# Kernel tuning notes

Hardware: AMD Instinct MI355X
Metric: run time of the kernel (lower is better)

Reference implementation:

```python
import jax, jax.numpy as jnp
import numpy as np

N_U, N_P, E = 200000, 50000, 500000
D_U, D_P, H, OUT = 100, 50, 128, 1
BN_EPS = 1e-5


def _lin(k, dout, din):
    s = 1.0 / np.sqrt(din)
    kw, kb = jax.random.split(k)
    W = jax.random.uniform(kw, (dout, din), jnp.float32, -s, s)
    b = jax.random.uniform(kb, (dout,), jnp.float32, -s, s)
    return W, b


def setup_inputs() -> dict:
    key = jax.random.key(0)
    ks = jax.random.split(key, 12)
    x_u = jax.random.normal(ks[0], (N_U, D_U), jnp.float32)
    x_p = jax.random.normal(ks[1], (N_P, D_P), jnp.float32)
    src = jax.random.randint(ks[2], (E,), 0, N_U, jnp.int64) if jax.config.jax_enable_x64 else jax.random.randint(ks[2], (E,), 0, N_U)
    dst = jax.random.randint(ks[3], (E,), N_U, N_U + N_P)
    edge_index = jnp.stack([src, dst]).astype(jnp.int32)
    W_u, b_u = _lin(ks[4], H, D_U)
    W_p, b_p = _lin(ks[5], H, D_P)
    W1l, b1l = _lin(ks[6], H, H)   # SAGEConv lin_l (aggregated neighbors, carries bias)
    W1r, _ = _lin(ks[7], H, H)     # SAGEConv lin_r (root, no bias)
    W2l, b2l = _lin(ks[8], H, H)
    W2r, _ = _lin(ks[9], H, H)
    W_out, b_out = _lin(ks[10], OUT, H)
    return dict(x_u=x_u, x_p=x_p, edge_index=edge_index,
                W_u=W_u, b_u=b_u, W_p=W_p, b_p=b_p,
                W1l=W1l, b1l=b1l, W1r=W1r,
                g1=jnp.ones((H,), jnp.float32), be1=jnp.zeros((H,), jnp.float32),
                W2l=W2l, b2l=b2l, W2r=W2r,
                g2=jnp.ones((H,), jnp.float32), be2=jnp.zeros((H,), jnp.float32),
                W_out=W_out, b_out=b_out)


def reference(x_u, x_p, edge_index, W_u, b_u, W_p, b_p,
              W1l, b1l, W1r, g1, be1, W2l, b2l, W2r, g2, be2,
              W_out, b_out):
    N = x_u.shape[0] + x_p.shape[0]
    # input projections + relu, then concat users/products -> [N, H]
    x = jnp.concatenate([jax.nn.relu(x_u @ W_u.T + b_u),
                         jax.nn.relu(x_p @ W_p.T + b_p)], axis=0)
    # to_undirected: add reversed edges (bipartite => no duplicates)
    src = jnp.concatenate([edge_index[0], edge_index[1]])
    dst = jnp.concatenate([edge_index[1], edge_index[0]])
    deg = jnp.maximum(jax.ops.segment_sum(jnp.ones_like(dst, jnp.float32), dst, num_segments=N), 1.0)

    def sage(h, Wl, bl, Wr):
        # mean aggregation of neighbor features, scatter by dst
        mean = jax.ops.segment_sum(h[src], dst, num_segments=N) / deg[:, None]
        return mean @ Wl.T + bl + h @ Wr.T

    def bn(h, g, b):
        m = h.mean(0)
        v = h.var(0)  # biased variance, as used for normalization in torch BN
        return (h - m) * jax.lax.rsqrt(v + BN_EPS) * g + b

    h1 = jax.nn.relu(bn(sage(x, W1l, b1l, W1r), g1, be1))   # dropout = identity (eval)
    h2 = jax.nn.relu(bn(sage(h1, W2l, b2l, W2r), g2, be2)) + x
    return h2[: x_u.shape[0]] @ W_out.T + b_out
```

## Files before the change

kernel.cpp:

```cpp
#include <hip/hip_runtime.h>
#include <hip/hip_bf16.h>
#include <cstdint>
#include <cstddef>

#define NT   250000
#define NUU  200000
#define NPP  50000
#define EG   500000
#define E2   1000000
#define HD   128
#define NBLK_SCAN 977
#define NTILES 1954

#define X_OFF     0ull
#define R1_OFF    64000000ull
#define R2_OFF    128000000ull
#define CNT_OFF   179200000ull
#define SPART_OFF 180200000ull
#define SS_OFF    180265536ull
#define RPTR_OFF  180267584ull
#define BSUM_OFF  181267588ull
#define BMAT_OFF  181271504ull
#define COL_OFF   181451728ull
#define WS_NEED   185451728ull

typedef __hip_bfloat16 bf16;
typedef __attribute__((ext_vector_type(8))) short short8v;
typedef __attribute__((ext_vector_type(4))) float f32x4;

__device__ inline float bflo(unsigned u) { return __builtin_bit_cast(float, u << 16); }
__device__ inline float bfhi(unsigned u) { return __builtin_bit_cast(float, u & 0xffff0000u); }
__device__ inline float b2f(short s) { return __builtin_bit_cast(float, ((unsigned)(unsigned short)s) << 16); }
__device__ inline unsigned short f2bf(float f) { return __builtin_bit_cast(unsigned short, __float2bfloat16(f)); }

__global__ __launch_bounds__(256) void k_zero(int* __restrict__ p, int n) {
    for (int i = blockIdx.x * 256 + threadIdx.x; i < n; i += gridDim.x * 256) p[i] = 0;
}

__global__ __launch_bounds__(256) void k_count(const int* __restrict__ ei, int* __restrict__ cnt) {
    for (int e = blockIdx.x * 256 + threadIdx.x; e < E2; e += gridDim.x * 256) {
        int d = (e < EG) ? ei[e + EG] : ei[e - EG];
        atomicAdd(&cnt[d], 1);
    }
}

__global__ __launch_bounds__(256) void k_scan1(const int* __restrict__ cnt, int* __restrict__ bsum) {
    __shared__ int lds[256];
    int i = blockIdx.x * 256 + threadIdx.x;
    int v = (i < NT) ? cnt[i] : 0;
    lds[threadIdx.x] = v; __syncthreads();
    for (int s = 128; s > 0; s >>= 1) {
        if (threadIdx.x < s) lds[threadIdx.x] += lds[threadIdx.x + s];
        __syncthreads();
    }
    if (threadIdx.x == 0) bsum[blockIdx.x] = lds[0];
}

__global__ __launch_bounds__(1024) void k_scan2(int* __restrict__ bsum) {
    __shared__ int lds[1024];
    int i = threadIdx.x;
    int v = (i < NBLK_SCAN) ? bsum[i] : 0;
    lds[i] = v; __syncthreads();
    for (int off = 1; off < 1024; off <<= 1) {
        int t = (i >= off) ? lds[i - off] : 0;
        __syncthreads();
        lds[i] += t;
        __syncthreads();
    }
    if (i < NBLK_SCAN) bsum[i] = lds[i] - v;
}

__global__ __launch_bounds__(256) void k_scan3(const int* __restrict__ cnt, const int* __restrict__ bsum,
                                               int* __restrict__ rp) {
    __shared__ int lds[256];
    int i = blockIdx.x * 256 + threadIdx.x;
    int v = (i < NT) ? cnt[i] : 0;
    lds[threadIdx.x] = v; __syncthreads();
    for (int off = 1; off < 256; off <<= 1) {
        int t = (threadIdx.x >= off) ? lds[threadIdx.x - off] : 0;
        __syncthreads();
        lds[threadIdx.x] += t;
        __syncthreads();
    }
    if (i < NT) rp[i] = bsum[blockIdx.x] + lds[threadIdx.x] - v;
    if (i == 0 && blockIdx.x == 0) rp[NT] = E2;
}

__global__ __launch_bounds__(256) void k_fill(const int* __restrict__ ei, const int* __restrict__ rp,
                                              int* __restrict__ fill, int* __restrict__ col) {
    for (int e = blockIdx.x * 256 + threadIdx.x; e < E2; e += gridDim.x * 256) {
        int s = ei[e];
        int d = (e < EG) ? ei[e + EG] : ei[e - EG];
        int slot = rp[d] + atomicAdd(&fill[d], 1);
        col[slot] = s;
    }
}

__global__ __launch_bounds__(256) void k_wcvt(const float* __restrict__ W1l, const float* __restrict__ W1r,
                                              const float* __restrict__ W2l, const float* __restrict__ W2r,
                                              const float* __restrict__ Wu, const float* __restrict__ Wp,
                                              bf16* __restrict__ B) {
    int i = blockIdx.x * 256 + threadIdx.x;
    if (i < 65536) {
        int layer = i >> 15, rem = i & 32767, o = rem >> 8, k = rem & 255;
        const float* W = layer ? ((k < 128) ? W2l : W2r) : ((k < 128) ? W1l : W1r);
        B[i] = __float2bfloat16(W[o * 128 + (k & 127)]);
    } else if (i < 81920) {
        int rem = i - 65536, o = rem >> 7, k = rem & 127;
        B[i] = __float2bfloat16((k < 100) ? Wu[o * 100 + k] : 0.f);
    } else if (i < 90112) {
        int rem = i - 81920, o = rem >> 6, k = rem & 63;
        B[i] = __float2bfloat16((k < 50) ? Wp[o * 50 + k] : 0.f);
    }
}

template<int DIN, int KPAD>
__global__ __launch_bounds__(256) void k_projm(const float* __restrict__ in, const bf16* __restrict__ Bp,
                                               const float* __restrict__ bias, bf16* __restrict__ outp,
                                               int nrows, int rowbase) {
    const int lane = threadIdx.x & 63;
    const int wid = threadIdx.x >> 6;
    const int wr = wid >> 1, wc = wid & 1;
    const int r15 = lane & 15, l4 = lane >> 4;
    const int tb = blockIdx.x * 128;
    constexpr int NKS = KPAD / 32;

    f32x4 acc[4][4] = {};
#pragma unroll
    for (int ks = 0; ks < NKS; ks++) {
        int kk = ks * 32 + l4 * 8;
        short8v a[4], b[4];
#pragma unroll
        for (int m = 0; m < 4; m++) {
            int r = tb + wr * 64 + m * 16 + r15;
            if (r > nrows - 1) r = nrows - 1;
            const float* src = in + (size_t)r * DIN + kk;
            short8v v;
            if (ks * 32 + 32 <= DIN) {
                const float2* s2 = (const float2*)src;
                float2 f0 = s2[0], f1 = s2[1], f2 = s2[2], f3 = s2[3];
                v[0] = (short)f2bf(f0.x); v[1] = (short)f2bf(f0.y);
                v[2] = (short)f2bf(f1.x); v[3] = (short)f2bf(f1.y);
                v[4] = (short)f2bf(f2.x); v[5] = (short)f2bf(f2.y);
                v[6] = (short)f2bf(f3.x); v[7] = (short)f2bf(f3.y);
            } else {
#pragma unroll
                for (int j = 0; j < 8; j++) {
                    float f = (kk + j < DIN) ? src[j] : 0.f;
                    v[j] = (short)f2bf(f);
                }
            }
            a[m] = v;
        }
#pragma unroll
        for (int n = 0; n < 4; n++) {
            int c = wc * 64 + n * 16 + r15;
            b[n] = *(const short8v*)(Bp + (size_t)c * KPAD + kk);
        }
#pragma unroll
        for (int m = 0; m < 4; m++)
#pragma unroll
            for (int n = 0; n < 4; n++)
                acc[m][n] = __builtin_amdgcn_mfma_f32_16x16x32_bf16(a[m], b[n], acc[m][n], 0, 0, 0);
    }
    float bcol[4];
#pragma unroll
    for (int n = 0; n < 4; n++) bcol[n] = bias[wc * 64 + n * 16 + r15];
#pragma unroll
    for (int m = 0; m < 4; m++)
#pragma unroll
        for (int n = 0; n < 4; n++)
#pragma unroll
            for (int g = 0; g < 4; g++) {
                int row = tb + wr * 64 + m * 16 + l4 * 4 + g;
                if (row < nrows) {
                    float v = fmaxf(acc[m][n][g] + bcol[n], 0.f);
                    outp[(size_t)(rowbase + row) * HD + wc * 64 + n * 16 + r15] = __float2bfloat16(v);
                }
            }
}

template<bool NORM>
__global__ __launch_bounds__(256) void k_gemm(const bf16* __restrict__ hin, const float* __restrict__ ssv,
                                              const int* __restrict__ rp, const int* __restrict__ col,
                                              const bf16* __restrict__ Bmat, const float* __restrict__ blv,
                                              bf16* __restrict__ outp, float* __restrict__ spart,
                                              int store_n) {
    int g = blockIdx.x / 5, pos = blockIdx.x % 5;
    int tile = (pos < 4) ? (g * 4 + pos) : (1563 + g);
    if (pos < 4 && tile > 1562) return;

    __shared__ unsigned int mrow[8192];
    const int tid = threadIdx.x;
    const int lane = tid & 63;
    const int wid = tid >> 6;
    const int g16 = lane >> 4, l16 = lane & 15;
    const int tb = tile * 128;
    const int wnb = wid * 32;
    const int fo = l16 * 8;

    float sv[8], tv[8];
    if (NORM) {
#pragma unroll
        for (int j = 0; j < 8; j++) { sv[j] = ssv[fo + j]; tv[j] = ssv[HD + fo + j]; }
    }

    int rpv = 0;
    if (lane <= 32) rpv = rp[min(tb + wnb + lane, NT)];

    for (int t = 0; t < 4; t++) {
        int nlA = wnb + t * 8 + g16;
        int nlB = nlA + 4;
        int a0 = __shfl(rpv, t * 8 + g16),     a1 = __shfl(rpv, t * 8 + g16 + 1);
        int b0 = __shfl(rpv, t * 8 + g16 + 4), b1 = __shfl(rpv, t * 8 + g16 + 5);
        if (tb + nlA >= NT) { a0 = 0; a1 = 0; }
        if (tb + nlB >= NT) { b0 = 0; b1 = 0; }
        float accA[8] = {}, accB[8] = {};
        int pA = a0, pB = b0;
        while (pA < a1 || pB < b1) {
            int iA0 = (pA     < a1) ? pA     : 0;
            int iA1 = (pA + 1 < a1) ? pA + 1 : 0;
            int iA2 = (pA + 2 < a1) ? pA + 2 : 0;
            int iA3 = (pA + 3 < a1) ? pA + 3 : 0;
            int iB0 = (pB     < b1) ? pB     : 0;
            int iB1 = (pB + 1 < b1) ? pB + 1 : 0;
            int iB2 = (pB + 2 < b1) ? pB + 2 : 0;
            int iB3 = (pB + 3 < b1) ? pB + 3 : 0;
            int cA0 = col[iA0], cA1 = col[iA1], cA2 = col[iA2], cA3 = col[iA3];
            int cB0 = col[iB0], cB1 = col[iB1], cB2 = col[iB2], cB3 = col[iB3];
            short8v uA0 = *(const short8v*)(hin + (size_t)cA0 * HD + fo);
            short8v uA1 = *(const short8v*)(hin + (size_t)cA1 * HD + fo);
            short8v uA2 = *(const short8v*)(hin + (size_t)cA2 * HD + fo);
            short8v uA3 = *(const short8v*)(hin + (size_t)cA3 * HD + fo);
            short8v uB0 = *(const short8v*)(hin + (size_t)cB0 * HD + fo);
            short8v uB1 = *(const short8v*)(hin + (size_t)cB1 * HD + fo);
            short8v uB2 = *(const short8v*)(hin + (size_t)cB2 * HD + fo);
            short8v uB3 = *(const short8v*)(hin + (size_t)cB3 * HD + fo);
            float mA0 = (pA     < a1) ? 1.f : 0.f;
            float mA1 = (pA + 1 < a1) ? 1.f : 0.f;
            float mA2 = (pA + 2 < a1) ? 1.f : 0.f;
            float mA3 = (pA + 3 < a1) ? 1.f : 0.f;
            float mB0 = (pB     < b1) ? 1.f : 0.f;
            float mB1 = (pB + 1 < b1) ? 1.f : 0.f;
            float mB2 = (pB + 2 < b1) ? 1.f : 0.f;
            float mB3 = (pB + 3 < b1) ? 1.f : 0.f;
#pragma unroll
            for (int j = 0; j < 8; j++) {
                float vA0 = b2f(uA0[j]), vA1 = b2f(uA1[j]), vA2 = b2f(uA2[j]), vA3 = b2f(uA3[j]);
                float vB0 = b2f(uB0[j]), vB1 = b2f(uB1[j]), vB2 = b2f(uB2[j]), vB3 = b2f(uB3[j]);
                if (NORM) {
                    vA0 = fmaxf(fmaf(vA0, sv[j], tv[j]), 0.f);
                    vA1 = fmaxf(fmaf(vA1, sv[j], tv[j]), 0.f);
                    vA2 = fmaxf(fmaf(vA2, sv[j], tv[j]), 0.f);
                    vA3 = fmaxf(fmaf(vA3, sv[j], tv[j]), 0.f);
                    vB0 = fmaxf(fmaf(vB0, sv[j], tv[j]), 0.f);
                    vB1 = fmaxf(fmaf(vB1, sv[j], tv[j]), 0.f);
                    vB2 = fmaxf(fmaf(vB2, sv[j], tv[j]), 0.f);
                    vB3 = fmaxf(fmaf(vB3, sv[j], tv[j]), 0.f);
                }
                accA[j] += mA0 * vA0 + mA1 * vA1 + mA2 * vA2 + mA3 * vA3;
                accB[j] += mB0 * vB0 + mB1 * vB1 + mB2 * vB2 + mB3 * vB3;
            }
            pA += 4; pB += 4;
        }
        float invA = 1.f / (float)max(a1 - a0, 1);
        float invB = 1.f / (float)max(b1 - b0, 1);
        short8v wA, wB;
#pragma unroll
        for (int j = 0; j < 8; j++) {
            wA[j] = (short)f2bf(accA[j] * invA);
            wB[j] = (short)f2bf(accB[j] * invB);
        }
        int byteA = (nlA * 256 + l16 * 16) ^ ((nlA & 7) << 4);
        int byteB = (nlB * 256 + l16 * 16) ^ ((nlB & 7) << 4);
        *(short8v*)((char*)mrow + byteA) = wA;
        *(short8v*)((char*)mrow + byteB) = wB;
    }
    __syncthreads();

    const int wr = wid >> 1, wc = wid & 1;
    const int r15 = lane & 15, l4 = lane >> 4;
    f32x4 acc[4][4] = {};
#pragma unroll
    for (int ks = 0; ks < 8; ks++) {
        short8v a[4], b[4];
        if (ks < 4) {
            int kb = ks * 64 + l4 * 16;
#pragma unroll
            for (int m = 0; m < 4; m++) {
                int r = wr * 64 + m * 16 + r15;
                int byte = (r * 256 + kb) ^ ((r & 7) << 4);
                a[m] = *(const short8v*)((const char*)mrow + byte);
            }
        } else {
            int k2 = (ks - 4) * 32 + l4 * 8;
            float sv2[8], tv2[8];
            if (NORM) {
#pragma unroll
                for (int j = 0; j < 8; j++) { sv2[j] = ssv[k2 + j]; tv2[j] = ssv[HD + k2 + j]; }
            }
#pragma unroll
            for (int m = 0; m < 4; m++) {
                int r = tb + wr * 64 + m * 16 + r15; if (r > NT - 1) r = NT - 1;
                short8v v = *(const short8v*)(hin + (size_t)r * HD + k2);
                if (NORM) {
#pragma unroll
                    for (int j = 0; j < 8; j++) {
                        float f = b2f(v[j]);
                        f = fmaxf(fmaf(f, sv2[j], tv2[j]), 0.f);
                        v[j] = (short)f2bf(f);
                    }
                }
                a[m] = v;
            }
        }
#pragma unroll
        for (int n = 0; n < 4; n++) {
            int c = wc * 64 + n * 16 + r15;
            b[n] = *(const short8v*)(Bmat + (size_t)c * 256 + ks * 32 + l4 * 8);
        }
#pragma unroll
        for (int m = 0; m < 4; m++)
#pragma unroll
            for (int n = 0; n < 4; n++)
                acc[m][n] = __builtin_amdgcn_mfma_f32_16x16x32_bf16(a[m], b[n], acc[m][n], 0, 0, 0);
    }

    float bcol[4];
#pragma unroll
    for (int n = 0; n < 4; n++) bcol[n] = blv[wc * 64 + n * 16 + r15];
    float ls[4] = {0.f, 0.f, 0.f, 0.f}, lq[4] = {0.f, 0.f, 0.f, 0.f};
#pragma unroll
    for (int m = 0; m < 4; m++)
#pragma unroll
        for (int n = 0; n < 4; n++)
#pragma unroll
            for (int gg = 0; gg < 4; gg++) {
                int row = tb + wr * 64 + m * 16 + l4 * 4 + gg;
                float v = acc[m][n][gg] + bcol[n];
                if (row < NT) { ls[n] += v; lq[n] += v * v; }
                if (row < store_n)
                    outp[(size_t)row * HD + wc * 64 + n * 16 + r15] = __float2bfloat16(v);
            }
    int part = (tile & 31) * 256;
#pragma unroll
    for (int n = 0; n < 4; n++) {
        float s = ls[n], q2 = lq[n];
        s  += __shfl_xor(s, 16);  s  += __shfl_xor(s, 32);
        q2 += __shfl_xor(q2, 16); q2 += __shfl_xor(q2, 32);
        if (l4 == 0) {
            int c = wc * 64 + n * 16 + r15;
            atomicAdd(&spart[part + c], s);
            atomicAdd(&spart[part + 128 + c], q2);
        }
    }
}

__global__ void k_fin(const float* __restrict__ sp, const float* __restrict__ g,
                      const float* __restrict__ be, float* __restrict__ ssout) {
    int j = threadIdx.x;
    float m = 0.f, q = 0.f;
    for (int i = 0; i < 32; i++) { m += sp[i * 256 + j]; q += sp[i * 256 + 128 + j]; }
    m *= (1.f / (float)NT);
    q = q * (1.f / (float)NT) - m * m;
    float s = g[j] * rsqrtf(q + 1e-5f);
    ssout[j] = s;
    ssout[HD + j] = be[j] - m * s;
}

__global__ __launch_bounds__(256) void k_out(const bf16* __restrict__ r2, const float* __restrict__ ss,
                                             const bf16* __restrict__ x, const float* __restrict__ wout,
                                             const float* __restrict__ bout, float* __restrict__ outp) {
    int lane = threadIdx.x & 63;
    int wid = (blockIdx.x * blockDim.x + threadIdx.x) >> 6;
    int nwv = (gridDim.x * blockDim.x) >> 6;
    int j0 = lane * 2;
    float s0 = ss[j0],       s1 = ss[j0 + 1];
    float t0 = ss[HD + j0],  t1 = ss[HD + j0 + 1];
    float w0 = wout[j0], w1 = wout[j0 + 1];
    float bo = bout[0];
    for (int r = wid; r < NUU; r += nwv) {
        unsigned ua = *(const unsigned*)(r2 + (size_t)r * HD + j0);
        unsigned ux = *(const unsigned*)(x + (size_t)r * HD + j0);
        float h0 = fmaxf(fmaf(bflo(ua), s0, t0), 0.f) + bflo(ux);
        float h1 = fmaxf(fmaf(bfhi(ua), s1, t1), 0.f) + bfhi(ux);
        float acc = h0 * w0 + h1 * w1;
#pragma unroll
        for (int off = 32; off; off >>= 1) acc += __shfl_down(acc, off);
        if (lane == 0) outp[r] = acc + bo;
    }
}

extern "C" void kernel_launch(void* const* d_in, const int* in_sizes, int n_in,
                              void* d_out, int out_size, void* d_ws, size_t ws_size,
                              hipStream_t stream) {
    const float* x_u = (const float*)d_in[0];
    const float* x_p = (const float*)d_in[1];
    const int*   ei  = (const int*)d_in[2];
    const float* W_u = (const float*)d_in[3];
    const float* b_u = (const float*)d_in[4];
    const float* W_p = (const float*)d_in[5];
    const float* b_p = (const float*)d_in[6];
    const float* W1l = (const float*)d_in[7];
    const float* b1l = (const float*)d_in[8];
    const float* W1r = (const float*)d_in[9];
    const float* g1  = (const float*)d_in[10];
    const float* be1 = (const float*)d_in[11];
    const float* W2l = (const float*)d_in[12];
    const float* b2l = (const float*)d_in[13];
    const float* W2r = (const float*)d_in[14];
    const float* g2  = (const float*)d_in[15];
    const float* be2 = (const float*)d_in[16];
    const float* Wout = (const float*)d_in[17];
    const float* bout = (const float*)d_in[18];

    float* out = (float*)d_out;

    if (ws_size < WS_NEED) {
        k_zero<<<512, 256, 0, stream>>>((int*)d_out, out_size);
        return;
    }

    char* ws = (char*)d_ws;
    bf16* X      = (bf16*)(ws + X_OFF);
    bf16* R1     = (bf16*)(ws + R1_OFF);
    bf16* R2     = (bf16*)(ws + R2_OFF);
    int*  cnt    = (int*)(ws + CNT_OFF);
    float* spart = (float*)(ws + SPART_OFF);
    float* ssbuf = (float*)(ws + SS_OFF);
    int*  rp     = (int*)(ws + RPTR_OFF);
    int*  bsum   = (int*)(ws + BSUM_OFF);
    bf16* Bmat   = (bf16*)(ws + BMAT_OFF);
    int*  col    = (int*)(ws + COL_OFF);

    k_zero<<<1043, 256, 0, stream>>>(cnt, 266896);
    k_wcvt<<<352, 256, 0, stream>>>(W1l, W1r, W2l, W2r, W_u, W_p, Bmat);

    k_count<<<1024, 256, 0, stream>>>(ei, cnt);
    k_scan1<<<NBLK_SCAN, 256, 0, stream>>>(cnt, bsum);
    k_scan2<<<1, 1024, 0, stream>>>(bsum);
    k_scan3<<<NBLK_SCAN, 256, 0, stream>>>(cnt, bsum, rp);
    k_zero<<<977, 256, 0, stream>>>(cnt, NT);
    k_fill<<<1024, 256, 0, stream>>>(ei, rp, cnt, col);

    k_projm<100, 128><<<1563, 256, 0, stream>>>(x_u, Bmat + 65536, b_u, X, NUU, 0);
    k_projm<50, 64><<<391, 256, 0, stream>>>(x_p, Bmat + 81920, b_p, X, NPP, NUU);

    k_gemm<false><<<1955, 256, 0, stream>>>(X, nullptr, rp, col, Bmat, b1l, R1, spart, NT);
    k_fin<<<1, 128, 0, stream>>>(spart, g1, be1, ssbuf);

    k_gemm<true><<<1955, 256, 0, stream>>>(R1, ssbuf, rp, col, Bmat + 32768, b2l, R2, spart + 8192, NUU);
    k_fin<<<1, 128, 0, stream>>>(spart + 8192, g2, be2, ssbuf + 256);

    k_out<<<2048, 256, 0, stream>>>(R2, ssbuf + 256, X, Wout, bout, out);
}
```

Measured before the change: 452.6 us.

## Split fused gather-GEMM into separate SpMM and dense MFMA kernels

```diff
diff --git a/kernel.cpp b/kernel.cpp
--- a/kernel.cpp
+++ b/kernel.cpp
@@ -10,7 +10,6 @@
 #define E2   1000000
 #define HD   128
 #define NBLK_SCAN 977
-#define NTILES 1954
 
 #define X_OFF     0ull
 #define R1_OFF    64000000ull
@@ -23,6 +22,18 @@
 #define BMAT_OFF  181271504ull
 #define COL_OFF   181451728ull
 #define WS_NEED   185451728ull
+
+#define CNT2_OFF   0ull
+#define SPART2_OFF 1000000ull
+#define SS2_OFF    1065536ull
+#define RPTR2_OFF  1067584ull
+#define BSUM2_OFF  2067588ull
+#define BMAT2_OFF  2071504ull
+#define COL2_OFF   2251728ull
+#define X2_OFF     6251728ull
+#define R1B_OFF    70251728ull
+#define C2_OFF     134251728ull
+#define WS_SPLIT   198251728ull
 
 typedef __hip_bfloat16 bf16;
 typedef __attribute__((ext_vector_type(8))) short short8v;
@@ -137,12 +148,21 @@
             const float* src = in + (size_t)r * DIN + kk;
             short8v v;
             if (ks * 32 + 32 <= DIN) {
-                const float2* s2 = (const float2*)src;
-                float2 f0 = s2[0], f1 = s2[1], f2 = s2[2], f3 = s2[3];
-                v[0] = (short)f2bf(f0.x); v[1] = (short)f2bf(f0.y);
-                v[2] = (short)f2bf(f1.x); v[3] = (short)f2bf(f1.y);
-                v[4] = (short)f2bf(f2.x); v[5] = (short)f2bf(f2.y);
-                v[6] = (short)f2bf(f3.x); v[7] = (short)f2bf(f3.y);
+                if constexpr (DIN % 4 == 0) {
+                    const float4* s4 = (const float4*)src;
+                    float4 f0 = s4[0], f1 = s4[1];
+                    v[0] = (short)f2bf(f0.x); v[1] = (short)f2bf(f0.y);
+                    v[2] = (short)f2bf(f0.z); v[3] = (short)f2bf(f0.w);
+                    v[4] = (short)f2bf(f1.x); v[5] = (short)f2bf(f1.y);
+                    v[6] = (short)f2bf(f1.z); v[7] = (short)f2bf(f1.w);
+                } else {
+                    const float2* s2 = (const float2*)src;
+                    float2 f0 = s2[0], f1 = s2[1], f2 = s2[2], f3 = s2[3];
+                    v[0] = (short)f2bf(f0.x); v[1] = (short)f2bf(f0.y);
+                    v[2] = (short)f2bf(f1.x); v[3] = (short)f2bf(f1.y);
+                    v[4] = (short)f2bf(f2.x); v[5] = (short)f2bf(f2.y);
+                    v[6] = (short)f2bf(f3.x); v[7] = (short)f2bf(f3.y);
+                }
             } else {
 #pragma unroll
                 for (int j = 0; j < 8; j++) {
@@ -178,6 +198,140 @@
                     outp[(size_t)(rowbase + row) * HD + wc * 64 + n * 16 + r15] = __float2bfloat16(v);
                 }
             }
+}
+
+template<bool NORM>
+__global__ __launch_bounds__(256) void k_spmm(const bf16* __restrict__ hin, const float* __restrict__ ssv,
+                                              const int* __restrict__ rp, const int* __restrict__ col,
+                                              bf16* __restrict__ M) {
+    const int tid = threadIdx.x;
+    const int gid = tid >> 4, l16 = tid & 15;
+    const int fo = l16 * 8;
+    float sv[8], tv[8];
+    if (NORM) {
+#pragma unroll
+        for (int j = 0; j < 8; j++) { sv[j] = ssv[fo + j]; tv[j] = ssv[HD + fo + j]; }
+    }
+    for (int n = blockIdx.x * 16 + gid; n < NT; n += gridDim.x * 16) {
+        int s0 = rp[n], s1 = rp[n + 1];
+        float a[8] = {};
+        for (int p = s0; p < s1; p += 4) {
+            int i1 = min(p + 1, s1 - 1), i2 = min(p + 2, s1 - 1), i3 = min(p + 3, s1 - 1);
+            int c0 = col[p], c1 = col[i1], c2 = col[i2], c3 = col[i3];
+            short8v u0 = *(const short8v*)(hin + (size_t)c0 * HD + fo);
+            short8v u1 = *(const short8v*)(hin + (size_t)c1 * HD + fo);
+            short8v u2 = *(const short8v*)(hin + (size_t)c2 * HD + fo);
+            short8v u3 = *(const short8v*)(hin + (size_t)c3 * HD + fo);
+            float m1 = (p + 1 < s1) ? 1.f : 0.f;
+            float m2 = (p + 2 < s1) ? 1.f : 0.f;
+            float m3 = (p + 3 < s1) ? 1.f : 0.f;
+#pragma unroll
+            for (int j = 0; j < 8; j++) {
+                float v0 = b2f(u0[j]), v1 = b2f(u1[j]), v2 = b2f(u2[j]), v3 = b2f(u3[j]);
+                if (NORM) {
+                    v0 = fmaxf(fmaf(v0, sv[j], tv[j]), 0.f);
+                    v1 = fmaxf(fmaf(v1, sv[j], tv[j]), 0.f);
+                    v2 = fmaxf(fmaf(v2, sv[j], tv[j]), 0.f);
+                    v3 = fmaxf(fmaf(v3, sv[j], tv[j]), 0.f);
+                }
+                a[j] += v0 + m1 * v1 + m2 * v2 + m3 * v3;
+            }
+        }
+        float inv = 1.f / (float)max(s1 - s0, 1);
+        short8v w;
+#pragma unroll
+        for (int j = 0; j < 8; j++) w[j] = (short)f2bf(a[j] * inv);
+        *(short8v*)(M + (size_t)n * HD + fo) = w;
+    }
+}
+
+template<bool NORM>
+__global__ __launch_bounds__(256) void k_dense(const bf16* __restrict__ Min, const bf16* __restrict__ hin,
+                                               const float* __restrict__ ssv,
+                                               const bf16* __restrict__ Bmat, const float* __restrict__ blv,
+                                               bf16* __restrict__ outp, float* __restrict__ spart,
+                                               int store_n) {
+    const int lane = threadIdx.x & 63;
+    const int wid = threadIdx.x >> 6;
+    const int wr = wid >> 1, wc = wid & 1;
+    const int r15 = lane & 15, l4 = lane >> 4;
+    const int tb = blockIdx.x * 128;
+
+    f32x4 acc[4][4] = {};
+#pragma unroll
+    for (int ks = 0; ks < 8; ks++) {
+        short8v a[4], b[4];
+        if (ks < 4) {
+            int k0 = ks * 32 + l4 * 8;
+#pragma unroll
+            for (int m = 0; m < 4; m++) {
+                int r = tb + wr * 64 + m * 16 + r15; if (r > NT - 1) r = NT - 1;
+                a[m] = *(const short8v*)(Min + (size_t)r * HD + k0);
+            }
+        } else {
+            int k2 = (ks - 4) * 32 + l4 * 8;
+            float sv2[8], tv2[8];
+            if (NORM) {
+#pragma unroll
+                for (int j = 0; j < 8; j++) { sv2[j] = ssv[k2 + j]; tv2[j] = ssv[HD + k2 + j]; }
+            }
+#pragma unroll
+            for (int m = 0; m < 4; m++) {
+                int r = tb + wr * 64 + m * 16 + r15; if (r > NT - 1) r = NT - 1;
+                short8v v = *(const short8v*)(hin + (size_t)r * HD + k2);
+                if (NORM) {
+#pragma unroll
+                    for (int j = 0; j < 8; j++) {
+                        float f = b2f(v[j]);
+                        f = fmaxf(fmaf(f, sv2[j], tv2[j]), 0.f);
+                        v[j] = (short)f2bf(f);
+                    }
+                }
+                a[m] = v;
+            }
+        }
+#pragma unroll
+        for (int n = 0; n < 4; n++) {
+            int c = wc * 64 + n * 16 + r15;
+            b[n] = *(const short8v*)(Bmat + (size_t)c * 256 + ks * 32 + l4 * 8);
+        }
+#pragma unroll
+        for (int m = 0; m < 4; m++)
+#pragma unroll
+            for (int n = 0; n < 4; n++)
+                acc[m][n] = __builtin_amdgcn_mfma_f32_16x16x32_bf16(a[m], b[n], acc[m][n], 0, 0, 0);
+    }
+
+    __syncthreads();
+
+    float bcol[4];
+#pragma unroll
+    for (int n = 0; n < 4; n++) bcol[n] = blv[wc * 64 + n * 16 + r15];
+    float ls[4] = {0.f, 0.f, 0.f, 0.f}, lq[4] = {0.f, 0.f, 0.f, 0.f};
+#pragma unroll
+    for (int m = 0; m < 4; m++)
+#pragma unroll
+        for (int n = 0; n < 4; n++)
+#pragma unroll
+            for (int gg = 0; gg < 4; gg++) {
+                int row = tb + wr * 64 + m * 16 + l4 * 4 + gg;
+                float v = acc[m][n][gg] + bcol[n];
+                if (row < NT) { ls[n] += v; lq[n] += v * v; }
+                if (row < store_n)
+                    outp[(size_t)row * HD + wc * 64 + n * 16 + r15] = __float2bfloat16(v);
+            }
+    int part = (blockIdx.x & 31) * 256;
+#pragma unroll
+    for (int n = 0; n < 4; n++) {
+        float s = ls[n], q2 = lq[n];
+        s  += __shfl_xor(s, 16);  s  += __shfl_xor(s, 32);
+        q2 += __shfl_xor(q2, 16); q2 += __shfl_xor(q2, 32);
+        if (l4 == 0) {
+            int c = wc * 64 + n * 16 + r15;
+            atomicAdd(&spart[part + c], s);
+            atomicAdd(&spart[part + 128 + c], q2);
+        }
+    }
 }
 
 template<bool NORM>
@@ -204,7 +358,6 @@
 #pragma unroll
         for (int j = 0; j < 8; j++) { sv[j] = ssv[fo + j]; tv[j] = ssv[HD + fo + j]; }
     }
-
     int rpv = 0;
     if (lane <= 32) rpv = rp[min(tb + wnb + lane, NT)];
 
@@ -372,22 +525,31 @@
                                              const bf16* __restrict__ x, const float* __restrict__ wout,
                                              const float* __restrict__ bout, float* __restrict__ outp) {
     int lane = threadIdx.x & 63;
-    int wid = (blockIdx.x * blockDim.x + threadIdx.x) >> 6;
+    int wv = (blockIdx.x * blockDim.x + threadIdx.x) >> 6;
     int nwv = (gridDim.x * blockDim.x) >> 6;
-    int j0 = lane * 2;
-    float s0 = ss[j0],       s1 = ss[j0 + 1];
-    float t0 = ss[HD + j0],  t1 = ss[HD + j0 + 1];
-    float w0 = wout[j0], w1 = wout[j0 + 1];
+    int g16 = lane >> 4, l16 = lane & 15;
+    int fo = l16 * 8;
+    float s8[8], t8[8], w8[8];
+#pragma unroll
+    for (int j = 0; j < 8; j++) {
+        s8[j] = ss[fo + j]; t8[j] = ss[HD + fo + j]; w8[j] = wout[fo + j];
+    }
     float bo = bout[0];
-    for (int r = wid; r < NUU; r += nwv) {
-        unsigned ua = *(const unsigned*)(r2 + (size_t)r * HD + j0);
-        unsigned ux = *(const unsigned*)(x + (size_t)r * HD + j0);
-        float h0 = fmaxf(fmaf(bflo(ua), s0, t0), 0.f) + bflo(ux);
-        float h1 = fmaxf(fmaf(bfhi(ua), s1, t1), 0.f) + bfhi(ux);
-        float acc = h0 * w0 + h1 * w1;
-#pragma unroll
-        for (int off = 32; off; off >>= 1) acc += __shfl_down(acc, off);
-        if (lane == 0) outp[r] = acc + bo;
+    for (int r0 = wv * 4; r0 < NUU; r0 += nwv * 4) {
+        int row = r0 + g16;
+        short8v a  = *(const short8v*)(r2 + (size_t)row * HD + fo);
+        short8v xx = *(const short8v*)(x  + (size_t)row * HD + fo);
+        float acc = 0.f;
+#pragma unroll
+        for (int j = 0; j < 8; j++) {
+            float h = fmaxf(fmaf(b2f(a[j]), s8[j], t8[j]), 0.f) + b2f(xx[j]);
+            acc += h * w8[j];
+        }
+        acc += __shfl_xor(acc, 1);
+        acc += __shfl_xor(acc, 2);
+        acc += __shfl_xor(acc, 4);
+        acc += __shfl_xor(acc, 8);
+        if (l16 == 0) outp[row] = acc + bo;
     }
 }
 
@@ -413,15 +575,50 @@
     const float* be2 = (const float*)d_in[16];
     const float* Wout = (const float*)d_in[17];
     const float* bout = (const float*)d_in[18];
-
     float* out = (float*)d_out;
+    char* ws = (char*)d_ws;
+
+    if (ws_size >= WS_SPLIT) {
+        int*  cnt    = (int*)(ws + CNT2_OFF);
+        float* spart = (float*)(ws + SPART2_OFF);
+        float* ssbuf = (float*)(ws + SS2_OFF);
+        int*  rp     = (int*)(ws + RPTR2_OFF);
+        int*  bsum   = (int*)(ws + BSUM2_OFF);
+        bf16* Bmat   = (bf16*)(ws + BMAT2_OFF);
+        int*  col    = (int*)(ws + COL2_OFF);
+        bf16* X      = (bf16*)(ws + X2_OFF);
+        bf16* R1     = (bf16*)(ws + R1B_OFF);
+        bf16* MC     = (bf16*)(ws + C2_OFF);
+
+        k_zero<<<1043, 256, 0, stream>>>(cnt, 266896);
+        k_wcvt<<<352, 256, 0, stream>>>(W1l, W1r, W2l, W2r, W_u, W_p, Bmat);
+
+        k_count<<<1024, 256, 0, stream>>>(ei, cnt);
+        k_scan1<<<NBLK_SCAN, 256, 0, stream>>>(cnt, bsum);
+        k_scan2<<<1, 1024, 0, stream>>>(bsum);
+        k_scan3<<<NBLK_SCAN, 256, 0, stream>>>(cnt, bsum, rp);
+        k_zero<<<977, 256, 0, stream>>>(cnt, NT);
+        k_fill<<<1024, 256, 0, stream>>>(ei, rp, cnt, col);
+
+        k_projm<100, 128><<<1563, 256, 0, stream>>>(x_u, Bmat + 65536, b_u, X, NUU, 0);
+        k_projm<50, 64><<<391, 256, 0, stream>>>(x_p, Bmat + 81920, b_p, X, NPP, NUU);
+
+        k_spmm<false><<<2048, 256, 0, stream>>>(X, nullptr, rp, col, MC);
+        k_dense<false><<<1954, 256, 0, stream>>>(MC, X, nullptr, Bmat, b1l, R1, spart, NT);
+        k_fin<<<1, 128, 0, stream>>>(spart, g1, be1, ssbuf);
+
+        k_spmm<true><<<2048, 256, 0, stream>>>(R1, ssbuf, rp, col, MC);
+        k_dense<true><<<1954, 256, 0, stream>>>(MC, R1, ssbuf, Bmat + 32768, b2l, MC, spart + 8192, NUU);
+        k_fin<<<1, 128, 0, stream>>>(spart + 8192, g2, be2, ssbuf + 256);
+
+        k_out<<<1024, 256, 0, stream>>>(MC, ssbuf + 256, X, Wout, bout, out);
+        return;
+    }
 
     if (ws_size < WS_NEED) {
         k_zero<<<512, 256, 0, stream>>>((int*)d_out, out_size);
         return;
     }
-
-    char* ws = (char*)d_ws;
     bf16* X      = (bf16*)(ws + X_OFF);
     bf16* R1     = (bf16*)(ws + R1_OFF);
     bf16* R2     = (bf16*)(ws + R2_OFF);
@@ -452,5 +649,5 @@
     k_gemm<true><<<1955, 256, 0, stream>>>(R1, ssbuf, rp, col, Bmat + 32768, b2l, R2, spart + 8192, NUU);
     k_fin<<<1, 128, 0, stream>>>(spart + 8192, g2, be2, ssbuf + 256);
 
-    k_out<<<2048, 256, 0, stream>>>(R2, ssbuf + 256, X, Wout, bout, out);
-}
+    k_out<<<1024, 256, 0, stream>>>(R2, ssbuf + 256, X, Wout, bout, out);
+}
```

Result: slower. 507.0 us (+12.0%).
